# Kernel tuning notes

Hardware: AMD Instinct MI355X
Metric: run time of the kernel (lower is better)

## Reference

```python
import jax, jax.numpy as jnp
import numpy as np
import math

B, N, F_IN, F_OUT = 2, 2048, 32, 32
R, LEV = 2, 2
SIGMA = 1.0


def setup_inputs() -> dict:
    key = jax.random.key(0)
    k1, k2, k3, k4 = jax.random.split(key, 4)
    x = jax.random.normal(k1, (B, N, F_IN), dtype=jnp.float32)
    # framelet decomposition operator, scaled so bmm outputs stay O(1)
    d_list = jax.random.normal(k2, (B, R * LEV * N, N + 1), dtype=jnp.float32) * (1.0 / math.sqrt(N))
    weight = jax.random.normal(k3, (F_IN, F_OUT), dtype=jnp.float32) * math.sqrt(2.0 / (F_IN + F_OUT))
    filt = jax.random.uniform(k4, (R * LEV * N, 1), dtype=jnp.float32, minval=0.9, maxval=1.1)
    bias = jnp.zeros((F_OUT,), dtype=jnp.float32)
    return {"x": x, "d_list": d_list, "weight": weight, "filt": filt, "bias": bias}


def reference(x, d_list, weight, filt, bias):
    num_nodes = x.shape[1]
    # dense feature transform
    xw = jnp.einsum('bnf,fo->bno', x, weight)
    # analysis: drop first column of d_list, bmm with transformed features
    y = d_list[:, :, 1:]                       # [B, r*Lev*N, N]
    xc = jnp.einsum('bmn,bno->bmo', y, xw)     # [B, r*Lev*N, F_OUT]
    xc = filt[None, :, :] * xc                 # learned diagonal filter
    # In the original, ms_idx is reset to 0 every loop iteration, so only
    # ms[0] (== 1.0 by construction in multiScales) is ever used as the scale.
    thr = math.sqrt(2.0 * math.log(num_nodes)) / math.sqrt(num_nodes) * SIGMA
    low = xc[:, (LEV - 1) * num_nodes:LEV * num_nodes, :]   # low-pass block, kept
    high = xc[:, LEV * num_nodes:, :]                        # high-freq blocks
    # soft threshold: sign(x)*(|x|-thr+||x|-thr|)/2 == sign(x)*relu(|x|-thr)
    high = jnp.sign(high) * jnp.maximum(jnp.abs(high) - thr, jnp.float32(0.0))
    x_shrink = jnp.concatenate([low, high], axis=1)          # [B, (r*Lev-1)*N, F_OUT]
    # synthesis: crop first node-block, raw reshape (not transpose!) as in original
    d_crop = d_list[:, num_nodes:, :]                        # [B, (r*Lev-1)*N, N+1]
    y2 = d_crop.reshape(d_crop.shape[0], num_nodes + 1, -1)  # [B, N+1, (r*Lev-1)*N]
    out = jnp.einsum('bkm,bmo->bko', y2, x_shrink) + bias    # [B, N+1, F_OUT]
    return out
```

## Files before the change

### kernel.cpp

```cpp
#include <hip/hip_runtime.h>
#include <math.h>


#define NB   2
#define NN   2048
#define DP   2049
#define M1   6144
#define OUTR 2049
#define KC   64
#define TM   16

#define XW_OFF 0
#define XS_OFF 131072

__device__ __forceinline__ void cp4(const float* g, float* l) {
  __builtin_amdgcn_global_load_lds((const __attribute__((address_space(1))) void*)g,
                                   (__attribute__((address_space(3))) void*)l, 4, 0, 0);
}
__device__ __forceinline__ void cp16(const float* g, float* l) {
  __builtin_amdgcn_global_load_lds((const __attribute__((address_space(1))) void*)g,
                                   (__attribute__((address_space(3))) void*)l, 16, 0, 0);
}

__global__ __launch_bounds__(256) void k_pre(const float* __restrict__ x,
                                             const float* __restrict__ wgt,
                                             const float* __restrict__ bias,
                                             float* __restrict__ xw_b,
                                             float* __restrict__ out) {
  const int bid = blockIdx.x, tid = threadIdx.x;
  if (bid < 512) {
    const int b = bid >> 8, tile = bid & 255;
    const int n = tile * 8 + (tid >> 5), o = tid & 31;
    const float* xr = x + ((size_t)b * NN + n) * 32;
    float acc = 0.f;
#pragma unroll
    for (int f = 0; f < 32; ++f) acc = fmaf(xr[f], wgt[f * 32 + o], acc);
    xw_b[((b * 512 + (n >> 2)) * 32 + o) * 4 + (n & 3)] = acc;
  } else {
    const int idx = (bid - 512) * 256 + tid;
    if (idx < NB * OUTR * 32) out[idx] = bias[idx & 31];
  }
}

__global__ __launch_bounds__(256) void k_pass1(const float* __restrict__ dlist,
                                               const float* __restrict__ xw_b,
                                               const float* __restrict__ filt,
                                               float* __restrict__ xs_b) {
  __shared__ float dl[2][TM][KC];
  __shared__ float xl[2][16][128];

  const int bid = blockIdx.x;
  const int b = bid / 384, tile = bid % 384;
  const int row0 = tile * TM;
  const int tid = threadIdx.x, w = tid >> 6, lane = tid & 63;
  const int o = lane & 31, g = lane >> 5;

  const float* dbase = dlist + ((size_t)(b * 8192 + 2048 + row0)) * DP + 1;
  const float* xwb = xw_b + b * 65536;

  auto stage = [&](int buf, int k0) {
#pragma unroll
    for (int i = 0; i < 4; ++i) {
      const int r = w * 4 + i;
      cp4(dbase + (size_t)r * DP + k0 + lane, &dl[buf][r][0]);
    }
#pragma unroll
    for (int i = 0; i < 2; ++i) {
      const int inst = w * 2 + i;
      cp16(xwb + k0 * 32 + inst * 256 + lane * 4, &xl[buf][0][0] + inst * 256);
    }
  };

  float acc0 = 0.f, acc1 = 0.f;
  const int r0 = w * 4 + g * 2, r1 = r0 + 1;

  stage(0, 0);
#pragma unroll 1
  for (int c = 0; c < 32; ++c) {
    __syncthreads();
    if (c + 1 < 32) stage((c + 1) & 1, (c + 1) * KC);
    const int buf = c & 1;
#pragma unroll
    for (int k4 = 0; k4 < 16; ++k4) {
      const float4 xq = *(const float4*)&xl[buf][k4][o * 4];
      const float4 d0 = *(const float4*)&dl[buf][r0][k4 * 4];
      const float4 d1 = *(const float4*)&dl[buf][r1][k4 * 4];
      acc0 = fmaf(d0.x, xq.x, acc0); acc0 = fmaf(d0.y, xq.y, acc0);
      acc0 = fmaf(d0.z, xq.z, acc0); acc0 = fmaf(d0.w, xq.w, acc0);
      acc1 = fmaf(d1.x, xq.x, acc1); acc1 = fmaf(d1.y, xq.y, acc1);
      acc1 = fmaf(d1.z, xq.z, acc1); acc1 = fmaf(d1.w, xq.w, acc1);
    }
  }

  const float THR = 0.08628973f;
  const int   m[2] = {row0 + r0, row0 + r1};
  const float a[2] = {acc0, acc1};
#pragma unroll
  for (int i = 0; i < 2; ++i) {
    float v = a[i] * filt[2048 + m[i]];
    if (m[i] >= 2048) {
      const float t = fabsf(v) - THR;
      v = t > 0.f ? copysignf(t, v) : 0.f;
    }
    xs_b[((size_t)(b * 1536 + (m[i] >> 2)) * 32 + o) * 4 + (m[i] & 3)] = v;
  }
}

__global__ __launch_bounds__(256) void k_pass2(const float* __restrict__ dlist,
                                               const float* __restrict__ xs_b,
                                               float* __restrict__ out) {
  __shared__ float dl[2][TM][KC];
  __shared__ float xl[2][16][128];

  const int tile = blockIdx.x, b = blockIdx.y, seg = blockIdx.z;
  const int row0 = tile * TM;
  const int m0 = seg * 2048;
  const int tid = threadIdx.x, w = tid >> 6, lane = tid & 63;
  const int o = lane & 31, g = lane >> 5;

  const float* ybase = dlist + (size_t)b * 8192 * DP + (size_t)2048 * DP + m0;
  const float* xsb = xs_b + b * 196608 + m0 * 32;

  auto stage = [&](int buf, int k0) {
    {
      const int rloc = w * 4 + (lane >> 4);
      int rg = row0 + rloc; if (rg > 2048) rg = 2048;
      cp16(ybase + (size_t)rg * 6144 + k0 + (lane & 15) * 4, &dl[buf][w * 4][0]);
    }
#pragma unroll
    for (int i = 0; i < 2; ++i) {
      const int inst = w * 2 + i;
      cp16(xsb + k0 * 32 + inst * 256 + lane * 4, &xl[buf][0][0] + inst * 256);
    }
  };

  float acc0 = 0.f, acc1 = 0.f;
  const int r0 = w * 4 + g * 2, r1 = r0 + 1;

  stage(0, 0);
#pragma unroll 1
  for (int c = 0; c < 32; ++c) {
    __syncthreads();
    if (c + 1 < 32) stage((c + 1) & 1, (c + 1) * KC);
    const int buf = c & 1;
#pragma unroll
    for (int k4 = 0; k4 < 16; ++k4) {
      const float4 xq = *(const float4*)&xl[buf][k4][o * 4];
      const float4 d0 = *(const float4*)&dl[buf][r0][k4 * 4];
      const float4 d1 = *(const float4*)&dl[buf][r1][k4 * 4];
      acc0 = fmaf(d0.x, xq.x, acc0); acc0 = fmaf(d0.y, xq.y, acc0);
      acc0 = fmaf(d0.z, xq.z, acc0); acc0 = fmaf(d0.w, xq.w, acc0);
      acc1 = fmaf(d1.x, xq.x, acc1); acc1 = fmaf(d1.y, xq.y, acc1);
      acc1 = fmaf(d1.z, xq.z, acc1); acc1 = fmaf(d1.w, xq.w, acc1);
    }
  }

  const int   k[2] = {row0 + r0, row0 + r1};
  const float a[2] = {acc0, acc1};
#pragma unroll
  for (int i = 0; i < 2; ++i)
    if (k[i] <= 2048)
      atomicAdd(&out[((size_t)b * OUTR + k[i]) * 32 + o], a[i]);
}

extern "C" void kernel_launch(void* const* d_in, const int* in_sizes, int n_in,
                              void* d_out, int out_size, void* d_ws, size_t ws_size,
                              hipStream_t stream) {
  const float* x     = (const float*)d_in[0];
  const float* dlist = (const float*)d_in[1];
  const float* wgt   = (const float*)d_in[2];
  const float* filt  = (const float*)d_in[3];
  const float* bias  = (const float*)d_in[4];
  float* out = (float*)d_out;
  float* ws  = (float*)d_ws;
  float* xw_b = ws + XW_OFF;
  float* xs_b = ws + XS_OFF;

  k_pre<<<dim3(1025), dim3(256), 0, stream>>>(x, wgt, bias, xw_b, out);
  k_pass1<<<dim3(768), dim3(256), 0, stream>>>(dlist, xw_b, filt, xs_b);
  k_pass2<<<dim3(129, 2, 3), dim3(256), 0, stream>>>(dlist, xs_b, out);
}
```

Baseline: 296.7 us.

## Restructure both GEMM passes with 128-row register tiles and split-K partial reductions

Both matrix passes now use 128-row tiles with a 4x4 per-thread register micro-tile and XOR-swizzled LDS staging. The right-hand operand is read straight from global memory instead of being staged in LDS. The K dimension is split across grid z, and partial sums go to workspace buffers. New shrink and reduce kernels sum those partials, and the reduce kernel replaces the atomic accumulation and the bias pre-fill. The aim is more FMA reuse per loaded element and no atomics, at the cost of extra workspace traffic and two more kernel launches.

```diff
diff --git a/kernel.cpp b/kernel.cpp
--- a/kernel.cpp
+++ b/kernel.cpp
@@ -2,16 +2,13 @@
 #include <math.h>
 
 
-#define NB   2
-#define NN   2048
-#define DP   2049
-#define M1   6144
-#define OUTR 2049
-#define KC   64
-#define TM   16
+#define DP 2049
+#define THRS 0.08628973f
 
 #define XW_OFF 0
 #define XS_OFF 131072
+#define P1_OFF 524288
+#define P2_OFF 3670016
 
 __device__ __forceinline__ void cp4(const float* g, float* l) {
   __builtin_amdgcn_global_load_lds((const __attribute__((address_space(1))) void*)g,
@@ -24,143 +21,196 @@
 
 __global__ __launch_bounds__(256) void k_pre(const float* __restrict__ x,
                                              const float* __restrict__ wgt,
-                                             const float* __restrict__ bias,
-                                             float* __restrict__ xw_b,
-                                             float* __restrict__ out) {
-  const int bid = blockIdx.x, tid = threadIdx.x;
-  if (bid < 512) {
-    const int b = bid >> 8, tile = bid & 255;
-    const int n = tile * 8 + (tid >> 5), o = tid & 31;
-    const float* xr = x + ((size_t)b * NN + n) * 32;
-    float acc = 0.f;
-#pragma unroll
-    for (int f = 0; f < 32; ++f) acc = fmaf(xr[f], wgt[f * 32 + o], acc);
-    xw_b[((b * 512 + (n >> 2)) * 32 + o) * 4 + (n & 3)] = acc;
-  } else {
-    const int idx = (bid - 512) * 256 + tid;
-    if (idx < NB * OUTR * 32) out[idx] = bias[idx & 31];
-  }
+                                             float* __restrict__ xw) {
+  const int gid = blockIdx.x * 256 + threadIdx.x;
+  const int r = gid >> 3, c0 = (gid & 7) * 4;
+  const float* xr = x + (size_t)r * 32;
+  float4 acc = {0.f, 0.f, 0.f, 0.f};
+#pragma unroll
+  for (int f = 0; f < 32; ++f) {
+    const float xv = xr[f];
+    const float4 wv = *(const float4*)(wgt + f * 32 + c0);
+    acc.x = fmaf(xv, wv.x, acc.x); acc.y = fmaf(xv, wv.y, acc.y);
+    acc.z = fmaf(xv, wv.z, acc.z); acc.w = fmaf(xv, wv.w, acc.w);
+  }
+  *(float4*)(xw + (size_t)r * 32 + c0) = acc;
 }
 
 __global__ __launch_bounds__(256) void k_pass1(const float* __restrict__ dlist,
-                                               const float* __restrict__ xw_b,
+                                               const float* __restrict__ xw,
                                                const float* __restrict__ filt,
-                                               float* __restrict__ xs_b) {
-  __shared__ float dl[2][TM][KC];
-  __shared__ float xl[2][16][128];
-
-  const int bid = blockIdx.x;
-  const int b = bid / 384, tile = bid % 384;
-  const int row0 = tile * TM;
-  const int tid = threadIdx.x, w = tid >> 6, lane = tid & 63;
-  const int o = lane & 31, g = lane >> 5;
-
-  const float* dbase = dlist + ((size_t)(b * 8192 + 2048 + row0)) * DP + 1;
-  const float* xwb = xw_b + b * 65536;
-
-  auto stage = [&](int buf, int k0) {
-#pragma unroll
-    for (int i = 0; i < 4; ++i) {
-      const int r = w * 4 + i;
-      cp4(dbase + (size_t)r * DP + k0 + lane, &dl[buf][r][0]);
-    }
-#pragma unroll
-    for (int i = 0; i < 2; ++i) {
-      const int inst = w * 2 + i;
-      cp16(xwb + k0 * 32 + inst * 256 + lane * 4, &xl[buf][0][0] + inst * 256);
+                                               float* __restrict__ p1) {
+  __shared__ float dl[2][4096];
+  const int tile = blockIdx.x;
+  const int b    = blockIdx.y;
+  const int s    = blockIdx.z;
+  const int tid = threadIdx.x, wv = tid >> 6, lane = tid & 63;
+  const int r_t = tid >> 3, c_t = tid & 7;
+  const int r0 = r_t * 4, c0 = c_t * 4, swzr = r_t & 7;
+
+  const int k_seg = s * 256;
+  const float* dbase = dlist + ((size_t)b * 8192 + 2048 + tile * 128) * DP + 1 + k_seg;
+  const float* xwb   = xw + ((size_t)b * 2048 + k_seg) * 32;
+
+  const int rhalf = lane >> 5, j = lane & 31, j16 = j >> 2, jrem = j & 3;
+  const float* sbase = dbase + (size_t)(wv * 32 + rhalf) * DP + jrem;
+
+  auto stage = [&](int buf, int kc) {
+    float* lb = &dl[buf][wv * 1024];
+#pragma unroll
+    for (int ii = 0; ii < 16; ++ii) {
+      const int scol = ((j16 ^ ((ii >> 1) & 7)) << 2);
+      cp4(sbase + kc + (size_t)(2 * ii) * DP + scol, lb + ii * 64);
     }
   };
 
-  float acc0 = 0.f, acc1 = 0.f;
-  const int r0 = w * 4 + g * 2, r1 = r0 + 1;
+  float4 acc[4];
+#pragma unroll
+  for (int i = 0; i < 4; ++i) acc[i] = {0.f, 0.f, 0.f, 0.f};
 
   stage(0, 0);
 #pragma unroll 1
-  for (int c = 0; c < 32; ++c) {
+  for (int c = 0; c < 8; ++c) {
     __syncthreads();
-    if (c + 1 < 32) stage((c + 1) & 1, (c + 1) * KC);
-    const int buf = c & 1;
-#pragma unroll
-    for (int k4 = 0; k4 < 16; ++k4) {
-      const float4 xq = *(const float4*)&xl[buf][k4][o * 4];
-      const float4 d0 = *(const float4*)&dl[buf][r0][k4 * 4];
-      const float4 d1 = *(const float4*)&dl[buf][r1][k4 * 4];
-      acc0 = fmaf(d0.x, xq.x, acc0); acc0 = fmaf(d0.y, xq.y, acc0);
-      acc0 = fmaf(d0.z, xq.z, acc0); acc0 = fmaf(d0.w, xq.w, acc0);
-      acc1 = fmaf(d1.x, xq.x, acc1); acc1 = fmaf(d1.y, xq.y, acc1);
-      acc1 = fmaf(d1.z, xq.z, acc1); acc1 = fmaf(d1.w, xq.w, acc1);
-    }
-  }
-
-  const float THR = 0.08628973f;
-  const int   m[2] = {row0 + r0, row0 + r1};
-  const float a[2] = {acc0, acc1};
-#pragma unroll
-  for (int i = 0; i < 2; ++i) {
-    float v = a[i] * filt[2048 + m[i]];
-    if (m[i] >= 2048) {
-      const float t = fabsf(v) - THR;
-      v = t > 0.f ? copysignf(t, v) : 0.f;
-    }
-    xs_b[((size_t)(b * 1536 + (m[i] >> 2)) * 32 + o) * 4 + (m[i] & 3)] = v;
+    if (c < 7) stage((c + 1) & 1, (c + 1) * 32);
+    const float* dbuf = &dl[c & 1][0];
+    const float* xwc  = xwb + (size_t)c * 32 * 32;
+#pragma unroll
+    for (int k4 = 0; k4 < 8; ++k4) {
+      const float4 w0 = *(const float4*)(xwc + (k4 * 4 + 0) * 32 + c0);
+      const float4 w1 = *(const float4*)(xwc + (k4 * 4 + 1) * 32 + c0);
+      const float4 w2 = *(const float4*)(xwc + (k4 * 4 + 2) * 32 + c0);
+      const float4 w3 = *(const float4*)(xwc + (k4 * 4 + 3) * 32 + c0);
+      const int colf = ((k4 ^ swzr) << 2);
+#pragma unroll
+      for (int i = 0; i < 4; ++i) {
+        const float4 d = *(const float4*)(dbuf + (r0 + i) * 32 + colf);
+        float4& a = acc[i];
+        a.x = fmaf(d.x, w0.x, a.x); a.y = fmaf(d.x, w0.y, a.y); a.z = fmaf(d.x, w0.z, a.z); a.w = fmaf(d.x, w0.w, a.w);
+        a.x = fmaf(d.y, w1.x, a.x); a.y = fmaf(d.y, w1.y, a.y); a.z = fmaf(d.y, w1.z, a.z); a.w = fmaf(d.y, w1.w, a.w);
+        a.x = fmaf(d.z, w2.x, a.x); a.y = fmaf(d.z, w2.y, a.y); a.z = fmaf(d.z, w2.z, a.z); a.w = fmaf(d.z, w2.w, a.w);
+        a.x = fmaf(d.w, w3.x, a.x); a.y = fmaf(d.w, w3.y, a.y); a.z = fmaf(d.w, w3.z, a.z); a.w = fmaf(d.w, w3.w, a.w);
+      }
+    }
+  }
+
+  const size_t pbase = ((size_t)(s * 2 + b) * 6144 + tile * 128) * 32;
+#pragma unroll
+  for (int i = 0; i < 4; ++i) {
+    const int m = tile * 128 + r0 + i;
+    const float fl = filt[2048 + m];
+    float4 v = acc[i];
+    v.x *= fl; v.y *= fl; v.z *= fl; v.w *= fl;
+    *(float4*)(p1 + pbase + (size_t)(r0 + i) * 32 + c0) = v;
+  }
+}
+
+__global__ __launch_bounds__(256) void k_shrink(const float* __restrict__ p1,
+                                                float* __restrict__ xs) {
+  const int q0 = blockIdx.x * 1024 + threadIdx.x;
+#pragma unroll
+  for (int t = 0; t < 4; ++t) {
+    const int f4 = q0 + t * 256;
+    const int row = f4 >> 3;
+    const int bb = row / 6144;
+    const int m  = row - bb * 6144;
+    float4 sum = {0.f, 0.f, 0.f, 0.f};
+#pragma unroll
+    for (int s = 0; s < 8; ++s) {
+      const float4 v = *(const float4*)(p1 + ((size_t)((s * 2 + bb) * 6144 + m) * 8 + (f4 & 7)) * 4);
+      sum.x += v.x; sum.y += v.y; sum.z += v.z; sum.w += v.w;
+    }
+    if (m >= 2048) {
+      float t0;
+      t0 = fabsf(sum.x) - THRS; sum.x = t0 > 0.f ? copysignf(t0, sum.x) : 0.f;
+      t0 = fabsf(sum.y) - THRS; sum.y = t0 > 0.f ? copysignf(t0, sum.y) : 0.f;
+      t0 = fabsf(sum.z) - THRS; sum.z = t0 > 0.f ? copysignf(t0, sum.z) : 0.f;
+      t0 = fabsf(sum.w) - THRS; sum.w = t0 > 0.f ? copysignf(t0, sum.w) : 0.f;
+    }
+    *(float4*)(xs + (size_t)f4 * 4) = sum;
   }
 }
 
 __global__ __launch_bounds__(256) void k_pass2(const float* __restrict__ dlist,
-                                               const float* __restrict__ xs_b,
-                                               float* __restrict__ out) {
-  __shared__ float dl[2][TM][KC];
-  __shared__ float xl[2][16][128];
-
-  const int tile = blockIdx.x, b = blockIdx.y, seg = blockIdx.z;
-  const int row0 = tile * TM;
-  const int m0 = seg * 2048;
-  const int tid = threadIdx.x, w = tid >> 6, lane = tid & 63;
-  const int o = lane & 31, g = lane >> 5;
-
-  const float* ybase = dlist + (size_t)b * 8192 * DP + (size_t)2048 * DP + m0;
-  const float* xsb = xs_b + b * 196608 + m0 * 32;
-
-  auto stage = [&](int buf, int k0) {
-    {
-      const int rloc = w * 4 + (lane >> 4);
-      int rg = row0 + rloc; if (rg > 2048) rg = 2048;
-      cp16(ybase + (size_t)rg * 6144 + k0 + (lane & 15) * 4, &dl[buf][w * 4][0]);
-    }
-#pragma unroll
-    for (int i = 0; i < 2; ++i) {
-      const int inst = w * 2 + i;
-      cp16(xsb + k0 * 32 + inst * 256 + lane * 4, &xl[buf][0][0] + inst * 256);
+                                               const float* __restrict__ xs,
+                                               float* __restrict__ p2) {
+  __shared__ float dl[2][4096];
+  const int tile = blockIdx.x;
+  const int b    = blockIdx.y;
+  const int s    = blockIdx.z;
+  const int tid = threadIdx.x, wv = tid >> 6, lane = tid & 63;
+  const int r_t = tid >> 3, c_t = tid & 7;
+  const int r0 = r_t * 4, c0 = c_t * 4, swzr = r_t & 7;
+
+  const int m0 = s * 384;
+  const float* Abase = dlist + (size_t)b * 8192 * DP + (size_t)2048 * DP + m0;
+  const float* xsb   = xs + ((size_t)b * 6144 + m0) * 32;
+
+  const int rloc = lane >> 3, j16 = lane & 7;
+  auto stage = [&](int buf, int kc) {
+    float* lb = &dl[buf][wv * 1024];
+#pragma unroll
+    for (int ii = 0; ii < 4; ++ii) {
+      const int row_l = wv * 32 + ii * 8 + rloc;
+      const int swz = (row_l >> 2) & 7;
+      int rowg = tile * 128 + row_l;
+      rowg = rowg > 2048 ? 2048 : rowg;
+      cp16(Abase + (size_t)rowg * 6144 + kc + ((j16 ^ swz) << 2), lb + ii * 256);
     }
   };
 
-  float acc0 = 0.f, acc1 = 0.f;
-  const int r0 = w * 4 + g * 2, r1 = r0 + 1;
+  float4 acc[4];
+#pragma unroll
+  for (int i = 0; i < 4; ++i) acc[i] = {0.f, 0.f, 0.f, 0.f};
 
   stage(0, 0);
 #pragma unroll 1
-  for (int c = 0; c < 32; ++c) {
+  for (int c = 0; c < 12; ++c) {
     __syncthreads();
-    if (c + 1 < 32) stage((c + 1) & 1, (c + 1) * KC);
-    const int buf = c & 1;
-#pragma unroll
-    for (int k4 = 0; k4 < 16; ++k4) {
-      const float4 xq = *(const float4*)&xl[buf][k4][o * 4];
-      const float4 d0 = *(const float4*)&dl[buf][r0][k4 * 4];
-      const float4 d1 = *(const float4*)&dl[buf][r1][k4 * 4];
-      acc0 = fmaf(d0.x, xq.x, acc0); acc0 = fmaf(d0.y, xq.y, acc0);
-      acc0 = fmaf(d0.z, xq.z, acc0); acc0 = fmaf(d0.w, xq.w, acc0);
-      acc1 = fmaf(d1.x, xq.x, acc1); acc1 = fmaf(d1.y, xq.y, acc1);
-      acc1 = fmaf(d1.z, xq.z, acc1); acc1 = fmaf(d1.w, xq.w, acc1);
-    }
-  }
-
-  const int   k[2] = {row0 + r0, row0 + r1};
-  const float a[2] = {acc0, acc1};
-#pragma unroll
-  for (int i = 0; i < 2; ++i)
-    if (k[i] <= 2048)
-      atomicAdd(&out[((size_t)b * OUTR + k[i]) * 32 + o], a[i]);
+    if (c < 11) stage((c + 1) & 1, (c + 1) * 32);
+    const float* dbuf = &dl[c & 1][0];
+    const float* xsc  = xsb + (size_t)c * 32 * 32;
+#pragma unroll
+    for (int k4 = 0; k4 < 8; ++k4) {
+      const float4 w0 = *(const float4*)(xsc + (k4 * 4 + 0) * 32 + c0);
+      const float4 w1 = *(const float4*)(xsc + (k4 * 4 + 1) * 32 + c0);
+      const float4 w2 = *(const float4*)(xsc + (k4 * 4 + 2) * 32 + c0);
+      const float4 w3 = *(const float4*)(xsc + (k4 * 4 + 3) * 32 + c0);
+      const int colf = ((k4 ^ swzr) << 2);
+#pragma unroll
+      for (int i = 0; i < 4; ++i) {
+        const float4 d = *(const float4*)(dbuf + (r0 + i) * 32 + colf);
+        float4& a = acc[i];
+        a.x = fmaf(d.x, w0.x, a.x); a.y = fmaf(d.x, w0.y, a.y); a.z = fmaf(d.x, w0.z, a.z); a.w = fmaf(d.x, w0.w, a.w);
+        a.x = fmaf(d.y, w1.x, a.x); a.y = fmaf(d.y, w1.y, a.y); a.z = fmaf(d.y, w1.z, a.z); a.w = fmaf(d.y, w1.w, a.w);
+        a.x = fmaf(d.z, w2.x, a.x); a.y = fmaf(d.z, w2.y, a.y); a.z = fmaf(d.z, w2.z, a.z); a.w = fmaf(d.z, w2.w, a.w);
+        a.x = fmaf(d.w, w3.x, a.x); a.y = fmaf(d.w, w3.y, a.y); a.z = fmaf(d.w, w3.z, a.z); a.w = fmaf(d.w, w3.w, a.w);
+      }
+    }
+  }
+
+  const size_t pbase = ((size_t)(s * 2 + b) * 2176 + tile * 128) * 32;
+#pragma unroll
+  for (int i = 0; i < 4; ++i)
+    *(float4*)(p2 + pbase + (size_t)(r0 + i) * 32 + c0) = acc[i];
+}
+
+__global__ __launch_bounds__(256) void k_reduce(const float* __restrict__ p2,
+                                                const float* __restrict__ bias,
+                                                float* __restrict__ out) {
+  const int idx = blockIdx.x * 256 + threadIdx.x;
+  if (idx >= 32784) return;
+  const int row = idx >> 3;
+  const int bb = row / 2049;
+  const int k  = row - bb * 2049;
+  const int o4 = idx & 7;
+  float4 sum = *(const float4*)(bias + o4 * 4);
+#pragma unroll
+  for (int s = 0; s < 16; ++s) {
+    const float4 v = *(const float4*)(p2 + ((size_t)((s * 2 + bb) * 2176 + k) * 8 + o4) * 4);
+    sum.x += v.x; sum.y += v.y; sum.z += v.z; sum.w += v.w;
+  }
+  *(float4*)(out + (size_t)idx * 4) = sum;
 }
 
 extern "C" void kernel_launch(void* const* d_in, const int* in_sizes, int n_in,
@@ -173,10 +223,14 @@
   const float* bias  = (const float*)d_in[4];
   float* out = (float*)d_out;
   float* ws  = (float*)d_ws;
-  float* xw_b = ws + XW_OFF;
-  float* xs_b = ws + XS_OFF;
-
-  k_pre<<<dim3(1025), dim3(256), 0, stream>>>(x, wgt, bias, xw_b, out);
-  k_pass1<<<dim3(768), dim3(256), 0, stream>>>(dlist, xw_b, filt, xs_b);
-  k_pass2<<<dim3(129, 2, 3), dim3(256), 0, stream>>>(dlist, xs_b, out);
-}
+  float* xw = ws + XW_OFF;
+  float* xs = ws + XS_OFF;
+  float* p1 = ws + P1_OFF;
+  float* p2 = ws + P2_OFF;
+
+  k_pre   <<<dim3(128),       dim3(256), 0, stream>>>(x, wgt, xw);
+  k_pass1 <<<dim3(48, 2, 8),  dim3(256), 0, stream>>>(dlist, xw, filt, p1);
+  k_shrink<<<dim3(96),        dim3(256), 0, stream>>>(p1, xs);
+  k_pass2 <<<dim3(17, 2, 16), dim3(256), 0, stream>>>(dlist, xs, p2);
+  k_reduce<<<dim3(129),       dim3(256), 0, stream>>>(p2, bias, out);
+}
```

Measured after the change: 273.3 us. 7.9% less time.

## Use bf16x3 split MFMA for both GEMMs with split-K partial buffers

Applied to the files above, without the earlier changes.

Replaces the FP32 FMA LDS-tiled GEMMs with MFMA 32x32x16 bf16 instructions. Each fp32 operand is split into high and low bf16 halves, and three products are accumulated to keep near-fp32 accuracy. Operands are loaded straight from global memory with no LDS staging. Both passes now use split-K grids that write partial sums, followed by separate reduce kernels (shrink with threshold, and a final reduce with bias) instead of atomics. The goal is to shift the bandwidth- and FMA-bound matmuls onto the matrix cores, at the cost of extra launches, partial-buffer traffic and a small loss of precision.

```diff
diff --git a/kernel.cpp b/kernel.cpp
--- a/kernel.cpp
+++ b/kernel.cpp
@@ -2,165 +2,201 @@
 #include <math.h>
 
 
-#define NB   2
-#define NN   2048
-#define DP   2049
-#define M1   6144
-#define OUTR 2049
-#define KC   64
-#define TM   16
-
-#define XW_OFF 0
-#define XS_OFF 131072
-
-__device__ __forceinline__ void cp4(const float* g, float* l) {
-  __builtin_amdgcn_global_load_lds((const __attribute__((address_space(1))) void*)g,
-                                   (__attribute__((address_space(3))) void*)l, 4, 0, 0);
-}
-__device__ __forceinline__ void cp16(const float* g, float* l) {
-  __builtin_amdgcn_global_load_lds((const __attribute__((address_space(1))) void*)g,
-                                   (__attribute__((address_space(3))) void*)l, 16, 0, 0);
+#define DP 2049
+#define THRS 0.08628973f
+
+typedef float  f32x4  __attribute__((ext_vector_type(4)));
+typedef float  f32x16 __attribute__((ext_vector_type(16)));
+typedef short  s16x8  __attribute__((ext_vector_type(8)));
+typedef unsigned short u16;
+
+#define XWT_H 0u
+#define XWT_L 262144u
+#define XST_H 524288u
+#define XST_L 1310720u
+#define P1_B  2097152u
+#define P2_B  14680064u
+
+union U8 { unsigned u[4]; s16x8 v; };
+
+__device__ __forceinline__ unsigned cvtpk(float a, float b) {
+  unsigned r;
+  asm("v_cvt_pk_bf16_f32 %0, %1, %2" : "=v"(r) : "v"(a), "v"(b));
+  return r;
+}
+__device__ __forceinline__ void split2(float a0, float a1, unsigned& h, unsigned& l) {
+  h = cvtpk(a0, a1);
+  const float f0 = __uint_as_float(h << 16);
+  const float f1 = __uint_as_float(h & 0xFFFF0000u);
+  l = cvtpk(a0 - f0, a1 - f1);
+}
+__device__ __forceinline__ f32x4 ld4u(const float* p) {
+  f32x4 r; __builtin_memcpy(&r, p, 16); return r;
 }
 
 __global__ __launch_bounds__(256) void k_pre(const float* __restrict__ x,
                                              const float* __restrict__ wgt,
-                                             const float* __restrict__ bias,
-                                             float* __restrict__ xw_b,
-                                             float* __restrict__ out) {
-  const int bid = blockIdx.x, tid = threadIdx.x;
-  if (bid < 512) {
-    const int b = bid >> 8, tile = bid & 255;
-    const int n = tile * 8 + (tid >> 5), o = tid & 31;
-    const float* xr = x + ((size_t)b * NN + n) * 32;
-    float acc = 0.f;
-#pragma unroll
-    for (int f = 0; f < 32; ++f) acc = fmaf(xr[f], wgt[f * 32 + o], acc);
-    xw_b[((b * 512 + (n >> 2)) * 32 + o) * 4 + (n & 3)] = acc;
-  } else {
-    const int idx = (bid - 512) * 256 + tid;
-    if (idx < NB * OUTR * 32) out[idx] = bias[idx & 31];
-  }
-}
-
-__global__ __launch_bounds__(256) void k_pass1(const float* __restrict__ dlist,
-                                               const float* __restrict__ xw_b,
-                                               const float* __restrict__ filt,
-                                               float* __restrict__ xs_b) {
-  __shared__ float dl[2][TM][KC];
-  __shared__ float xl[2][16][128];
-
-  const int bid = blockIdx.x;
-  const int b = bid / 384, tile = bid % 384;
-  const int row0 = tile * TM;
-  const int tid = threadIdx.x, w = tid >> 6, lane = tid & 63;
-  const int o = lane & 31, g = lane >> 5;
-
-  const float* dbase = dlist + ((size_t)(b * 8192 + 2048 + row0)) * DP + 1;
-  const float* xwb = xw_b + b * 65536;
-
-  auto stage = [&](int buf, int k0) {
-#pragma unroll
-    for (int i = 0; i < 4; ++i) {
-      const int r = w * 4 + i;
-      cp4(dbase + (size_t)r * DP + k0 + lane, &dl[buf][r][0]);
+                                             u16* __restrict__ xwt_h,
+                                             u16* __restrict__ xwt_l) {
+  const int idx = blockIdx.x * 256 + threadIdx.x;
+  const int n0  = (idx & 255) * 8;
+  const int col = (idx >> 8) & 31;
+  const int b   = idx >> 13;
+  const float* xr = x + ((size_t)b * 2048 + n0) * 32;
+  float acc[8];
+#pragma unroll
+  for (int j = 0; j < 8; ++j) acc[j] = 0.f;
+#pragma unroll 8
+  for (int f = 0; f < 32; ++f) {
+    const float wf = wgt[f * 32 + col];
+#pragma unroll
+    for (int j = 0; j < 8; ++j) acc[j] = fmaf(xr[j * 32 + f], wf, acc[j]);
+  }
+  U8 H, L;
+#pragma unroll
+  for (int p = 0; p < 4; ++p) split2(acc[2 * p], acc[2 * p + 1], H.u[p], L.u[p]);
+  const size_t o = ((size_t)b * 32 + col) * 2048 + n0;
+  *(s16x8*)(xwt_h + o) = H.v;
+  *(s16x8*)(xwt_l + o) = L.v;
+}
+
+__global__ __launch_bounds__(256, 4) void k_pass1(const float* __restrict__ dlist,
+                                                  const u16* __restrict__ xwt_h,
+                                                  const u16* __restrict__ xwt_l,
+                                                  const float* __restrict__ filt,
+                                                  float* __restrict__ p1) {
+  const int mt = blockIdx.x, b = blockIdx.y, s = blockIdx.z;
+  const int tid = threadIdx.x, wv = tid >> 6, lane = tid & 63;
+  const int rc = lane & 31, oct = lane >> 5;
+  const int m_a = mt * 128 + wv * 32 + rc;
+  const int k0 = s * 256;
+
+  const float* A  = dlist + ((size_t)(b * 8192 + 2048 + m_a)) * DP + 1 + k0 + oct * 8;
+  const u16*   Bh = xwt_h + ((size_t)b * 32 + rc) * 2048 + k0 + oct * 8;
+  const u16*   Bl = xwt_l + ((size_t)b * 32 + rc) * 2048 + k0 + oct * 8;
+
+  f32x16 acc = {0.f,0.f,0.f,0.f,0.f,0.f,0.f,0.f,0.f,0.f,0.f,0.f,0.f,0.f,0.f,0.f};
+#pragma unroll 2
+  for (int st = 0; st < 16; ++st) {
+    const f32x4 a0 = ld4u(A + st * 16);
+    const f32x4 a1 = ld4u(A + st * 16 + 4);
+    U8 Ah, Al;
+    split2(a0.x, a0.y, Ah.u[0], Al.u[0]);
+    split2(a0.z, a0.w, Ah.u[1], Al.u[1]);
+    split2(a1.x, a1.y, Ah.u[2], Al.u[2]);
+    split2(a1.z, a1.w, Ah.u[3], Al.u[3]);
+    const s16x8 bh = *(const s16x8*)(Bh + st * 16);
+    const s16x8 bl = *(const s16x8*)(Bl + st * 16);
+    acc = __builtin_amdgcn_mfma_f32_32x32x16_bf16(Ah.v, bh, acc, 0, 0, 0);
+    acc = __builtin_amdgcn_mfma_f32_32x32x16_bf16(Al.v, bh, acc, 0, 0, 0);
+    acc = __builtin_amdgcn_mfma_f32_32x32x16_bf16(Ah.v, bl, acc, 0, 0, 0);
+  }
+
+  float* pc = p1 + ((size_t)((s * 2 + b) * 32 + rc)) * 6144 + mt * 128 + wv * 32 + 4 * oct;
+  const float* fb = filt + 2048 + mt * 128 + wv * 32 + 4 * oct;
+#pragma unroll
+  for (int g = 0; g < 4; ++g) {
+    const f32x4 fv = *(const f32x4*)(fb + 8 * g);
+    f32x4 v;
+    v.x = acc[4 * g + 0] * fv.x; v.y = acc[4 * g + 1] * fv.y;
+    v.z = acc[4 * g + 2] * fv.z; v.w = acc[4 * g + 3] * fv.w;
+    *(f32x4*)(pc + 8 * g) = v;
+  }
+}
+
+__global__ __launch_bounds__(256) void k_shrink(const float* __restrict__ p1,
+                                                u16* __restrict__ xst_h,
+                                                u16* __restrict__ xst_l) {
+  const int idx = blockIdx.x * 256 + threadIdx.x;
+  const int m0  = (idx % 768) * 8;
+  const int col = (idx / 768) % 32;
+  const int b   = idx / 24576;
+  f32x4 s0 = {0.f,0.f,0.f,0.f}, s1 = {0.f,0.f,0.f,0.f};
+#pragma unroll
+  for (int s = 0; s < 8; ++s) {
+    const float* pr = p1 + ((size_t)((s * 2 + b) * 32 + col)) * 6144 + m0;
+    const f32x4 v0 = *(const f32x4*)pr;
+    const f32x4 v1 = *(const f32x4*)(pr + 4);
+    s0 += v0; s1 += v1;
+  }
+  float a[8] = {s0.x, s0.y, s0.z, s0.w, s1.x, s1.y, s1.z, s1.w};
+  if (m0 >= 2048) {
+#pragma unroll
+    for (int j = 0; j < 8; ++j) {
+      const float t = fabsf(a[j]) - THRS;
+      a[j] = t > 0.f ? copysignf(t, a[j]) : 0.f;
     }
-#pragma unroll
-    for (int i = 0; i < 2; ++i) {
-      const int inst = w * 2 + i;
-      cp16(xwb + k0 * 32 + inst * 256 + lane * 4, &xl[buf][0][0] + inst * 256);
-    }
-  };
-
-  float acc0 = 0.f, acc1 = 0.f;
-  const int r0 = w * 4 + g * 2, r1 = r0 + 1;
-
-  stage(0, 0);
-#pragma unroll 1
-  for (int c = 0; c < 32; ++c) {
-    __syncthreads();
-    if (c + 1 < 32) stage((c + 1) & 1, (c + 1) * KC);
-    const int buf = c & 1;
-#pragma unroll
-    for (int k4 = 0; k4 < 16; ++k4) {
-      const float4 xq = *(const float4*)&xl[buf][k4][o * 4];
-      const float4 d0 = *(const float4*)&dl[buf][r0][k4 * 4];
-      const float4 d1 = *(const float4*)&dl[buf][r1][k4 * 4];
-      acc0 = fmaf(d0.x, xq.x, acc0); acc0 = fmaf(d0.y, xq.y, acc0);
-      acc0 = fmaf(d0.z, xq.z, acc0); acc0 = fmaf(d0.w, xq.w, acc0);
-      acc1 = fmaf(d1.x, xq.x, acc1); acc1 = fmaf(d1.y, xq.y, acc1);
-      acc1 = fmaf(d1.z, xq.z, acc1); acc1 = fmaf(d1.w, xq.w, acc1);
-    }
-  }
-
-  const float THR = 0.08628973f;
-  const int   m[2] = {row0 + r0, row0 + r1};
-  const float a[2] = {acc0, acc1};
-#pragma unroll
-  for (int i = 0; i < 2; ++i) {
-    float v = a[i] * filt[2048 + m[i]];
-    if (m[i] >= 2048) {
-      const float t = fabsf(v) - THR;
-      v = t > 0.f ? copysignf(t, v) : 0.f;
-    }
-    xs_b[((size_t)(b * 1536 + (m[i] >> 2)) * 32 + o) * 4 + (m[i] & 3)] = v;
-  }
-}
-
-__global__ __launch_bounds__(256) void k_pass2(const float* __restrict__ dlist,
-                                               const float* __restrict__ xs_b,
-                                               float* __restrict__ out) {
-  __shared__ float dl[2][TM][KC];
-  __shared__ float xl[2][16][128];
-
-  const int tile = blockIdx.x, b = blockIdx.y, seg = blockIdx.z;
-  const int row0 = tile * TM;
-  const int m0 = seg * 2048;
-  const int tid = threadIdx.x, w = tid >> 6, lane = tid & 63;
-  const int o = lane & 31, g = lane >> 5;
-
-  const float* ybase = dlist + (size_t)b * 8192 * DP + (size_t)2048 * DP + m0;
-  const float* xsb = xs_b + b * 196608 + m0 * 32;
-
-  auto stage = [&](int buf, int k0) {
-    {
-      const int rloc = w * 4 + (lane >> 4);
-      int rg = row0 + rloc; if (rg > 2048) rg = 2048;
-      cp16(ybase + (size_t)rg * 6144 + k0 + (lane & 15) * 4, &dl[buf][w * 4][0]);
-    }
-#pragma unroll
-    for (int i = 0; i < 2; ++i) {
-      const int inst = w * 2 + i;
-      cp16(xsb + k0 * 32 + inst * 256 + lane * 4, &xl[buf][0][0] + inst * 256);
-    }
-  };
-
-  float acc0 = 0.f, acc1 = 0.f;
-  const int r0 = w * 4 + g * 2, r1 = r0 + 1;
-
-  stage(0, 0);
-#pragma unroll 1
-  for (int c = 0; c < 32; ++c) {
-    __syncthreads();
-    if (c + 1 < 32) stage((c + 1) & 1, (c + 1) * KC);
-    const int buf = c & 1;
-#pragma unroll
-    for (int k4 = 0; k4 < 16; ++k4) {
-      const float4 xq = *(const float4*)&xl[buf][k4][o * 4];
-      const float4 d0 = *(const float4*)&dl[buf][r0][k4 * 4];
-      const float4 d1 = *(const float4*)&dl[buf][r1][k4 * 4];
-      acc0 = fmaf(d0.x, xq.x, acc0); acc0 = fmaf(d0.y, xq.y, acc0);
-      acc0 = fmaf(d0.z, xq.z, acc0); acc0 = fmaf(d0.w, xq.w, acc0);
-      acc1 = fmaf(d1.x, xq.x, acc1); acc1 = fmaf(d1.y, xq.y, acc1);
-      acc1 = fmaf(d1.z, xq.z, acc1); acc1 = fmaf(d1.w, xq.w, acc1);
-    }
-  }
-
-  const int   k[2] = {row0 + r0, row0 + r1};
-  const float a[2] = {acc0, acc1};
-#pragma unroll
-  for (int i = 0; i < 2; ++i)
-    if (k[i] <= 2048)
-      atomicAdd(&out[((size_t)b * OUTR + k[i]) * 32 + o], a[i]);
+  }
+  U8 H, L;
+#pragma unroll
+  for (int p = 0; p < 4; ++p) split2(a[2 * p], a[2 * p + 1], H.u[p], L.u[p]);
+  const size_t o = ((size_t)b * 32 + col) * 6144 + m0;
+  *(s16x8*)(xst_h + o) = H.v;
+  *(s16x8*)(xst_l + o) = L.v;
+}
+
+__global__ __launch_bounds__(256, 4) void k_pass2(const float* __restrict__ dlist,
+                                                  const u16* __restrict__ xst_h,
+                                                  const u16* __restrict__ xst_l,
+                                                  float* __restrict__ p2) {
+  const int kt = blockIdx.x, b = blockIdx.y, s = blockIdx.z;
+  const int tid = threadIdx.x, wv = tid >> 6, lane = tid & 63;
+  const int rc = lane & 31, oct = lane >> 5;
+  int krow = kt * 128 + wv * 32 + rc;
+  if (krow > 2048) krow = 2048;
+  const int m0 = s * 256;
+
+  const float* A  = dlist + (size_t)b * 8192 * DP + (size_t)2048 * DP
+                  + (size_t)krow * 6144 + m0 + oct * 8;
+  const u16*   Bh = xst_h + ((size_t)b * 32 + rc) * 6144 + m0 + oct * 8;
+  const u16*   Bl = xst_l + ((size_t)b * 32 + rc) * 6144 + m0 + oct * 8;
+
+  f32x16 acc = {0.f,0.f,0.f,0.f,0.f,0.f,0.f,0.f,0.f,0.f,0.f,0.f,0.f,0.f,0.f,0.f};
+#pragma unroll 2
+  for (int st = 0; st < 16; ++st) {
+    const f32x4 a0 = *(const f32x4*)(A + st * 16);
+    const f32x4 a1 = *(const f32x4*)(A + st * 16 + 4);
+    U8 Ah, Al;
+    split2(a0.x, a0.y, Ah.u[0], Al.u[0]);
+    split2(a0.z, a0.w, Ah.u[1], Al.u[1]);
+    split2(a1.x, a1.y, Ah.u[2], Al.u[2]);
+    split2(a1.z, a1.w, Ah.u[3], Al.u[3]);
+    const s16x8 bh = *(const s16x8*)(Bh + st * 16);
+    const s16x8 bl = *(const s16x8*)(Bl + st * 16);
+    acc = __builtin_amdgcn_mfma_f32_32x32x16_bf16(Ah.v, bh, acc, 0, 0, 0);
+    acc = __builtin_amdgcn_mfma_f32_32x32x16_bf16(Al.v, bh, acc, 0, 0, 0);
+    acc = __builtin_amdgcn_mfma_f32_32x32x16_bf16(Ah.v, bl, acc, 0, 0, 0);
+  }
+
+  float* pc = p2 + ((size_t)((s * 2 + b) * 32 + rc)) * 2176 + kt * 128 + wv * 32 + 4 * oct;
+#pragma unroll
+  for (int g = 0; g < 4; ++g) {
+    f32x4 v;
+    v.x = acc[4 * g + 0]; v.y = acc[4 * g + 1];
+    v.z = acc[4 * g + 2]; v.w = acc[4 * g + 3];
+    *(f32x4*)(pc + 8 * g) = v;
+  }
+}
+
+__global__ __launch_bounds__(256) void k_reduce(const float* __restrict__ p2,
+                                                const float* __restrict__ bias,
+                                                float* __restrict__ out) {
+  const int idx = blockIdx.x * 256 + threadIdx.x;
+  if (idx >= 34816) return;
+  const int k4  = idx % 544;
+  const int col = (idx / 544) % 32;
+  const int b   = idx / 17408;
+  const int k0r = k4 * 4;
+  f32x4 sum = {0.f,0.f,0.f,0.f};
+#pragma unroll 8
+  for (int s = 0; s < 24; ++s)
+    sum += *(const f32x4*)(p2 + ((size_t)((s * 2 + b) * 32 + col)) * 2176 + k0r);
+  const float bv = bias[col];
+#pragma unroll
+  for (int j = 0; j < 4; ++j) {
+    const int k = k0r + j;
+    if (k <= 2048) out[((size_t)b * 2049 + k) * 32 + col] = sum[j] + bv;
+  }
 }
 
 extern "C" void kernel_launch(void* const* d_in, const int* in_sizes, int n_in,
@@ -172,11 +208,17 @@
   const float* filt  = (const float*)d_in[3];
   const float* bias  = (const float*)d_in[4];
   float* out = (float*)d_out;
-  float* ws  = (float*)d_ws;
-  float* xw_b = ws + XW_OFF;
-  float* xs_b = ws + XS_OFF;
-
-  k_pre<<<dim3(1025), dim3(256), 0, stream>>>(x, wgt, bias, xw_b, out);
-  k_pass1<<<dim3(768), dim3(256), 0, stream>>>(dlist, xw_b, filt, xs_b);
-  k_pass2<<<dim3(129, 2, 3), dim3(256), 0, stream>>>(dlist, xs_b, out);
-}
+  char*  ws  = (char*)d_ws;
+  u16*   xwt_h = (u16*)(ws + XWT_H);
+  u16*   xwt_l = (u16*)(ws + XWT_L);
+  u16*   xst_h = (u16*)(ws + XST_H);
+  u16*   xst_l = (u16*)(ws + XST_L);
+  float* p1    = (float*)(ws + P1_B);
+  float* p2    = (float*)(ws + P2_B);
+
+  k_pre   <<<dim3(64),         dim3(256), 0, stream>>>(x, wgt, xwt_h, xwt_l);
+  k_pass1 <<<dim3(48, 2, 8),   dim3(256), 0, stream>>>(dlist, xwt_h, xwt_l, filt, p1);
+  k_shrink<<<dim3(192),        dim3(256), 0, stream>>>(p1, xst_h, xst_l);
+  k_pass2 <<<dim3(17, 2, 24),  dim3(256), 0, stream>>>(dlist, xst_h, xst_l, p2);
+  k_reduce<<<dim3(136),        dim3(256), 0, stream>>>(p2, bias, out);
+}
```

After: 269.5 us. 1.1x faster.
